# Kernel optimization log

Measured on AMD Instinct MI355X. Metric: run time of the kernel, lower is better.

The kernel has to match this reference:

```python
import jax, jax.numpy as jnp
import numpy as np

B, H, S, D = 2, 16, 2048, 64  # batch, heads, seq (n_qry == n_tok), head_dim


def setup_inputs() -> dict:
    key = jax.random.key(0)
    kq, kk, kv = jax.random.split(key, 3)
    Q = jax.random.normal(kq, (B, H, S, D), dtype=jnp.float32)
    K_cache = jax.random.normal(kk, (B, H, S, D), dtype=jnp.float32)
    V_cache = jax.random.normal(kv, (B, H, S, D), dtype=jnp.float32)
    return {"Q": Q, "K_cache": K_cache, "V_cache": V_cache}


def reference(Q, K_cache, V_cache):
    n_qry = Q.shape[-2]
    n_tok = K_cache.shape[-2]
    scale = 1.0 / jnp.sqrt(jnp.asarray(Q.shape[-1], Q.dtype))
    # [B, H, n_qry, n_tok] scores
    A = jnp.einsum('bhqd,bhkd->bhqk', Q, K_cache) * scale
    # causal mask: query q may attend key k iff k <= q + (n_tok - n_qry)
    q_idx = jnp.arange(n_qry)[:, None]
    k_idx = jnp.arange(n_tok)[None, :]
    mask = k_idx <= q_idx + (n_tok - n_qry)
    A = jnp.where(mask, A, -jnp.inf)
    P = jax.nn.softmax(A, axis=-1)
    return jnp.einsum('bhqk,bhkd->bhqd', P, V_cache)
```

## Files before the change

kernel.cpp:

```cpp
#include <hip/hip_runtime.h>

typedef __attribute__((ext_vector_type(8))) short bf16x8;
typedef __attribute__((ext_vector_type(4))) short bf16x4;
typedef __attribute__((ext_vector_type(4))) float f32x4;

#define NB 2
#define NH 16
#define NS 2048
#define ND 64
#define NBH (NB * NH)
#define QSCALE (0.125f * 1.44269504088896f)
#define CMAX 12.0f

static __device__ __forceinline__ unsigned pack2(float lo, float hi) {
  return __builtin_amdgcn_perm(__builtin_bit_cast(unsigned, hi),
                               __builtin_bit_cast(unsigned, lo), 0x07060302u);
}

__global__ __launch_bounds__(256) void prep_kernel(const float* __restrict__ K,
                                                   const float* __restrict__ V,
                                                   short* __restrict__ W) {
  const int bh = blockIdx.x >> 5, kb = blockIdx.x & 31;
  const float* Kp = K + (size_t)bh * NS * ND + (size_t)kb * 64 * ND;
  const float* Vp = V + (size_t)bh * NS * ND + (size_t)kb * 64 * ND;
  short* Wp = W + ((size_t)bh * 32 + kb) * 8192;

#pragma unroll
  for (int e0 = 0; e0 < 512; e0 += 256) {
    int e = e0 + threadIdx.x;
    int c = e >> 6, lane = e & 63;
    int st = c >> 1, cc = c & 1, quad = lane >> 4, col = lane & 15;
    const float* kr = Kp + (st * 16 + col) * ND + cc * 32 + quad * 8;
    float4 a = *(const float4*)kr;
    float4 b = *(const float4*)(kr + 4);
    uint4 u = {pack2(a.x, a.y), pack2(a.z, a.w), pack2(b.x, b.y), pack2(b.z, b.w)};
    *(uint4*)(Wp + (size_t)e * 8) = u;
  }
#pragma unroll
  for (int e0 = 0; e0 < 512; e0 += 256) {
    int e = e0 + threadIdx.x;
    int c = e >> 6, lane = e & 63;
    int st = c >> 1, th = c & 1, quad = lane >> 4, col = lane & 15;
    float f[8];
#pragma unroll
    for (int r = 0; r < 8; ++r) {
      int j = r & 3, t = th * 2 + (r >> 2);
      f[r] = Vp[(st * 16 + quad * 4 + j) * ND + t * 16 + col];
    }
    uint4 u = {pack2(f[0], f[1]), pack2(f[2], f[3]),
               pack2(f[4], f[5]), pack2(f[6], f[7])};
    *(uint4*)(Wp + 4096 + (size_t)e * 8) = u;
  }
}

__global__ __launch_bounds__(256) void fa_kernel(
    const float* __restrict__ Q, const short* __restrict__ W,
    float* __restrict__ O) {
  const int lane = threadIdx.x & 63;
  const int wave = threadIdx.x >> 6;
  const int col  = lane & 15;
  const int quad = lane >> 4;
  const int xcd  = blockIdx.x & 7;
  const int slot = blockIdx.x >> 3;
  const int bh   = xcd * 4 + (slot >> 4);
  const int pr   = slot & 15;
  const int stepsA = pr + 1;
  const int tileB  = 31 - pr;
  const int TOT = 33;

  __shared__ short Kbuf[2][4096];
  __shared__ short Vbuf[2][4096];

  const float* Qp = Q + (size_t)bh * NS * ND;
  const short* Wb = W + (size_t)bh * 32 * 8192;
  float*       Op = O + (size_t)bh * NS * ND;

  bf16x8 qf[2];
  f32x4 o4[4];
  float lsum;

  auto loadQ = [&](int qtile) {
    const float* qrow = Qp + (size_t)(qtile * 64 + wave * 16 + col) * ND + quad * 8;
#pragma unroll
    for (int c = 0; c < 2; ++c) {
      float4 a = *(const float4*)(qrow + c * 32);
      float4 b = *(const float4*)(qrow + c * 32 + 4);
      union { bf16x8 v; unsigned u[4]; } t;
      t.u[0] = pack2(a.x * QSCALE, a.y * QSCALE);
      t.u[1] = pack2(a.z * QSCALE, a.w * QSCALE);
      t.u[2] = pack2(b.x * QSCALE, b.y * QSCALE);
      t.u[3] = pack2(b.z * QSCALE, b.w * QSCALE);
      qf[c] = t.v;
    }
#pragma unroll
    for (int t = 0; t < 4; ++t) o4[t] = (f32x4){0.f, 0.f, 0.f, 0.f};
    lsum = 0.f;
  };

  auto stage = [&](int s, int b) {
    int kt = (s < stepsA) ? s : s - stepsA;
    const short* base = Wb + (size_t)kt * 8192;
#pragma unroll
    for (int i = 0; i < 4; ++i) {
      int id = wave * 4 + i;
      const short* g = base + id * 512 + lane * 8;
      __attribute__((address_space(3))) void* dst =
          (id < 8)
              ? (__attribute__((address_space(3))) void*)&Kbuf[b][id * 512]
              : (__attribute__((address_space(3))) void*)&Vbuf[b][(id - 8) * 512];
      __builtin_amdgcn_global_load_lds(
          (const __attribute__((address_space(1))) void*)g, dst, 16, 0, 0);
    }
  };

  auto epilogue = [&](int qtile) {
    float lt = lsum;
    lt += __shfl_xor(lt, 16, 64);
    lt += __shfl_xor(lt, 32, 64);
#pragma unroll
    for (int r = 0; r < 4; ++r) {
      float lr = __shfl(lt, quad * 4 + r, 64);
      float inv = 1.0f / lr;
      float* orow = Op + (size_t)(qtile * 64 + wave * 16 + quad * 4 + r) * ND + col;
#pragma unroll
      for (int t = 0; t < 4; ++t) orow[t * 16] = o4[t][r] * inv;
    }
  };

  loadQ(pr);
  stage(0, 0);
  __syncthreads();

  int qtile = pr;
  bool inB = false;
  for (int s = 0; s < TOT; ++s) {
    if (s + 1 < TOT) stage(s + 1, (s + 1) & 1);
    const int b = s & 1;
    const int local = inB ? (s - stepsA) : s;
    const int steps = inB ? (32 - pr) : stepsA;
    const bool last = (local == steps - 1);

    float sc[4][4];
#pragma unroll
    for (int st = 0; st < 4; ++st) {
      bf16x8 k0 = *(const bf16x8*)&Kbuf[b][(st * 2 + 0) * 512 + lane * 8];
      bf16x8 k1 = *(const bf16x8*)&Kbuf[b][(st * 2 + 1) * 512 + lane * 8];
      f32x4 acc = (f32x4){-CMAX, -CMAX, -CMAX, -CMAX};
      acc = __builtin_amdgcn_mfma_f32_16x16x32_bf16(k0, qf[0], acc, 0, 0, 0);
      acc = __builtin_amdgcn_mfma_f32_16x16x32_bf16(k1, qf[1], acc, 0, 0, 0);
#pragma unroll
      for (int r = 0; r < 4; ++r) sc[st][r] = acc[r];
    }
    if (last) {
      int qo = wave * 16 + col;
#pragma unroll
      for (int st = 0; st < 4; ++st)
#pragma unroll
        for (int r = 0; r < 4; ++r)
          if (st * 16 + quad * 4 + r > qo) sc[st][r] = -INFINITY;
    }

    bf16x4 pf[4];
#pragma unroll
    for (int st = 0; st < 4; ++st) {
      float p0 = __builtin_amdgcn_exp2f(sc[st][0]);
      float p1 = __builtin_amdgcn_exp2f(sc[st][1]);
      float p2 = __builtin_amdgcn_exp2f(sc[st][2]);
      float p3 = __builtin_amdgcn_exp2f(sc[st][3]);
      lsum += (p0 + p1) + (p2 + p3);
      union { bf16x4 v; unsigned u[2]; } tp;
      tp.u[0] = pack2(p0, p1);
      tp.u[1] = pack2(p2, p3);
      pf[st] = tp.v;
    }

#pragma unroll
    for (int st = 0; st < 4; ++st)
#pragma unroll
      for (int th = 0; th < 2; ++th) {
        bf16x8 vv = *(const bf16x8*)&Vbuf[b][(st * 2 + th) * 512 + lane * 8];
        bf16x4 vlo = __builtin_shufflevector(vv, vv, 0, 1, 2, 3);
        bf16x4 vhi = __builtin_shufflevector(vv, vv, 4, 5, 6, 7);
        o4[th * 2 + 0] =
            __builtin_amdgcn_mfma_f32_16x16x16bf16_1k(pf[st], vlo, o4[th * 2 + 0], 0, 0, 0);
        o4[th * 2 + 1] =
            __builtin_amdgcn_mfma_f32_16x16x16bf16_1k(pf[st], vhi, o4[th * 2 + 1], 0, 0, 0);
      }

    if (last) {
      epilogue(qtile);
      if (!inB) { inB = true; qtile = tileB; loadQ(tileB); }
    }
    __syncthreads();
  }
}

extern "C" void kernel_launch(void* const* d_in, const int* in_sizes, int n_in,
                              void* d_out, int out_size, void* d_ws, size_t ws_size,
                              hipStream_t stream) {
  const float* Q = (const float*)d_in[0];
  const float* K = (const float*)d_in[1];
  const float* V = (const float*)d_in[2];
  short* W = (short*)d_ws;
  hipLaunchKernelGGL(prep_kernel, dim3(NBH * 32), dim3(256), 0, stream, K, V, W);
  hipLaunchKernelGGL(fa_kernel, dim3(512), dim3(256), 0, stream, Q, W,
                     (float*)d_out);
}
```

Measured before the change: 123.6 us.

## Process paired query tiles concurrently per block with 16x16x32 PV MFMAs

Each block now runs its two causal query tiles concurrently: waves 0-1 handle the short tile and waves 2-3 the long tile. Each wave covers 32 query rows, so every K/V LDS fragment is reused across two MFMAs. The K and V workspace layout is permuted so the PV product can use 16x16x32 bf16 MFMAs instead of 16x16x16. V is transposed through padded shared memory in the prep kernel, and the grid is reordered into two phases with launch_bounds(256,2). The waves on the short tile sit idle after finishing, which trades load balance within a block for fewer loop steps and fewer LDS reads per FLOP.

```diff
diff --git a/kernel.cpp b/kernel.cpp
--- a/kernel.cpp
+++ b/kernel.cpp
@@ -1,14 +1,13 @@
 #include <hip/hip_runtime.h>
 
 typedef __attribute__((ext_vector_type(8))) short bf16x8;
-typedef __attribute__((ext_vector_type(4))) short bf16x4;
 typedef __attribute__((ext_vector_type(4))) float f32x4;
 
 #define NB 2
 #define NH 16
 #define NS 2048
 #define ND 64
-#define NBH (NB * NH)
+#define NBH 32
 #define QSCALE (0.125f * 1.44269504088896f)
 #define CMAX 12.0f
 
@@ -16,6 +15,7 @@
   return __builtin_amdgcn_perm(__builtin_bit_cast(unsigned, hi),
                                __builtin_bit_cast(unsigned, lo), 0x07060302u);
 }
+
 
 __global__ __launch_bounds__(256) void prep_kernel(const float* __restrict__ K,
                                                    const float* __restrict__ V,
@@ -25,48 +25,70 @@
   const float* Vp = V + (size_t)bh * NS * ND + (size_t)kb * 64 * ND;
   short* Wp = W + ((size_t)bh * 32 + kb) * 8192;
 
+  __shared__ float vt[64 * 65];
+
+  {
+    int vrow = threadIdx.x >> 2, seg = threadIdx.x & 3;
+    const float* src = Vp + vrow * ND + seg * 16;
+    float* dst = vt + vrow * 65 + seg * 16;
+#pragma unroll
+    for (int i = 0; i < 4; ++i) {
+      float4 v = *(const float4*)(src + i * 4);
+      dst[i * 4 + 0] = v.x; dst[i * 4 + 1] = v.y;
+      dst[i * 4 + 2] = v.z; dst[i * 4 + 3] = v.w;
+    }
+  }
+
 #pragma unroll
   for (int e0 = 0; e0 < 512; e0 += 256) {
     int e = e0 + threadIdx.x;
     int c = e >> 6, lane = e & 63;
     int st = c >> 1, cc = c & 1, quad = lane >> 4, col = lane & 15;
-    const float* kr = Kp + (st * 16 + col) * ND + cc * 32 + quad * 8;
+    int prow = 32 * (st >> 1) + 8 * (col >> 2) + 4 * (st & 1) + (col & 3);
+    const float* kr = Kp + prow * ND + cc * 32 + quad * 8;
     float4 a = *(const float4*)kr;
     float4 b = *(const float4*)(kr + 4);
     uint4 u = {pack2(a.x, a.y), pack2(a.z, a.w), pack2(b.x, b.y), pack2(b.z, b.w)};
     *(uint4*)(Wp + (size_t)e * 8) = u;
   }
+  __syncthreads();
+
 #pragma unroll
   for (int e0 = 0; e0 < 512; e0 += 256) {
     int e = e0 + threadIdx.x;
     int c = e >> 6, lane = e & 63;
-    int st = c >> 1, th = c & 1, quad = lane >> 4, col = lane & 15;
+    int g = c >> 2, t = c & 3, quad = lane >> 4, col = lane & 15;
+    const float* base = vt + (32 * g + 8 * quad) * 65 + t * 16 + col;
     float f[8];
 #pragma unroll
-    for (int r = 0; r < 8; ++r) {
-      int j = r & 3, t = th * 2 + (r >> 2);
-      f[r] = Vp[(st * 16 + quad * 4 + j) * ND + t * 16 + col];
-    }
+    for (int j = 0; j < 8; ++j) f[j] = base[j * 65];
     uint4 u = {pack2(f[0], f[1]), pack2(f[2], f[3]),
                pack2(f[4], f[5]), pack2(f[6], f[7])};
     *(uint4*)(Wp + 4096 + (size_t)e * 8) = u;
   }
 }
 
-__global__ __launch_bounds__(256) void fa_kernel(
+__global__ __launch_bounds__(256, 2) void fa_kernel(
     const float* __restrict__ Q, const short* __restrict__ W,
     float* __restrict__ O) {
   const int lane = threadIdx.x & 63;
   const int wave = threadIdx.x >> 6;
   const int col  = lane & 15;
   const int quad = lane >> 4;
-  const int xcd  = blockIdx.x & 7;
-  const int slot = blockIdx.x >> 3;
-  const int bh   = xcd * 4 + (slot >> 4);
-  const int pr   = slot & 15;
+
+  const int i = blockIdx.x;
+  const int phase = i >> 8;
+  const int rr_ = i & 255;
+  const int xcd = rr_ & 7;
+  const int s5 = rr_ >> 3;
+  const int bh = xcd * 4 + (s5 & 3);
+  const int pp = s5 >> 2;
+  const int pr = phase ? (15 - pp) : pp;
   const int stepsA = pr + 1;
-  const int tileB  = 31 - pr;
-  const int TOT = 33;
+  const int TOT = 32 - pr;
+  const int myTile  = (wave < 2) ? pr : (31 - pr);
+  const int mySteps = (wave < 2) ? stepsA : TOT;
+  const int qhalf = wave & 1;
 
   __shared__ short Kbuf[2][4096];
   __shared__ short Vbuf[2][4096];
@@ -75,12 +97,11 @@
   const short* Wb = W + (size_t)bh * 32 * 8192;
   float*       Op = O + (size_t)bh * NS * ND;
 
-  bf16x8 qf[2];
-  f32x4 o4[4];
-  float lsum;
-
-  auto loadQ = [&](int qtile) {
-    const float* qrow = Qp + (size_t)(qtile * 64 + wave * 16 + col) * ND + quad * 8;
+  bf16x8 qf[2][2];
+#pragma unroll
+  for (int f = 0; f < 2; ++f) {
+    const float* qrow =
+        Qp + (size_t)(myTile * 64 + qhalf * 32 + f * 16 + col) * ND + quad * 8;
 #pragma unroll
     for (int c = 0; c < 2; ++c) {
       float4 a = *(const float4*)(qrow + c * 32);
@@ -90,19 +111,22 @@
       t.u[1] = pack2(a.z * QSCALE, a.w * QSCALE);
       t.u[2] = pack2(b.x * QSCALE, b.y * QSCALE);
       t.u[3] = pack2(b.z * QSCALE, b.w * QSCALE);
-      qf[c] = t.v;
-    }
-#pragma unroll
-    for (int t = 0; t < 4; ++t) o4[t] = (f32x4){0.f, 0.f, 0.f, 0.f};
-    lsum = 0.f;
-  };
+      qf[f][c] = t.v;
+    }
+  }
+
+  f32x4 o4[2][4];
+#pragma unroll
+  for (int f = 0; f < 2; ++f)
+#pragma unroll
+    for (int t = 0; t < 4; ++t) o4[f][t] = (f32x4){0.f, 0.f, 0.f, 0.f};
+  float lsum[2] = {0.f, 0.f};
 
   auto stage = [&](int s, int b) {
-    int kt = (s < stepsA) ? s : s - stepsA;
-    const short* base = Wb + (size_t)kt * 8192;
-#pragma unroll
-    for (int i = 0; i < 4; ++i) {
-      int id = wave * 4 + i;
+    const short* base = Wb + (size_t)s * 8192;
+#pragma unroll
+    for (int ii = 0; ii < 4; ++ii) {
+      int id = wave * 4 + ii;
       const short* g = base + id * 512 + lane * 8;
       __attribute__((address_space(3))) void* dst =
           (id < 8)
@@ -113,83 +137,95 @@
     }
   };
 
-  auto epilogue = [&](int qtile) {
-    float lt = lsum;
-    lt += __shfl_xor(lt, 16, 64);
-    lt += __shfl_xor(lt, 32, 64);
-#pragma unroll
-    for (int r = 0; r < 4; ++r) {
-      float lr = __shfl(lt, quad * 4 + r, 64);
-      float inv = 1.0f / lr;
-      float* orow = Op + (size_t)(qtile * 64 + wave * 16 + quad * 4 + r) * ND + col;
-#pragma unroll
-      for (int t = 0; t < 4; ++t) orow[t * 16] = o4[t][r] * inv;
-    }
-  };
-
-  loadQ(pr);
   stage(0, 0);
   __syncthreads();
 
-  int qtile = pr;
-  bool inB = false;
   for (int s = 0; s < TOT; ++s) {
     if (s + 1 < TOT) stage(s + 1, (s + 1) & 1);
     const int b = s & 1;
-    const int local = inB ? (s - stepsA) : s;
-    const int steps = inB ? (32 - pr) : stepsA;
-    const bool last = (local == steps - 1);
-
-    float sc[4][4];
-#pragma unroll
-    for (int st = 0; st < 4; ++st) {
-      bf16x8 k0 = *(const bf16x8*)&Kbuf[b][(st * 2 + 0) * 512 + lane * 8];
-      bf16x8 k1 = *(const bf16x8*)&Kbuf[b][(st * 2 + 1) * 512 + lane * 8];
-      f32x4 acc = (f32x4){-CMAX, -CMAX, -CMAX, -CMAX};
-      acc = __builtin_amdgcn_mfma_f32_16x16x32_bf16(k0, qf[0], acc, 0, 0, 0);
-      acc = __builtin_amdgcn_mfma_f32_16x16x32_bf16(k1, qf[1], acc, 0, 0, 0);
-#pragma unroll
-      for (int r = 0; r < 4; ++r) sc[st][r] = acc[r];
-    }
-    if (last) {
-      int qo = wave * 16 + col;
-#pragma unroll
-      for (int st = 0; st < 4; ++st)
-#pragma unroll
-        for (int r = 0; r < 4; ++r)
-          if (st * 16 + quad * 4 + r > qo) sc[st][r] = -INFINITY;
-    }
-
-    bf16x4 pf[4];
-#pragma unroll
-    for (int st = 0; st < 4; ++st) {
-      float p0 = __builtin_amdgcn_exp2f(sc[st][0]);
-      float p1 = __builtin_amdgcn_exp2f(sc[st][1]);
-      float p2 = __builtin_amdgcn_exp2f(sc[st][2]);
-      float p3 = __builtin_amdgcn_exp2f(sc[st][3]);
-      lsum += (p0 + p1) + (p2 + p3);
-      union { bf16x4 v; unsigned u[2]; } tp;
-      tp.u[0] = pack2(p0, p1);
-      tp.u[1] = pack2(p2, p3);
-      pf[st] = tp.v;
-    }
-
-#pragma unroll
-    for (int st = 0; st < 4; ++st)
-#pragma unroll
-      for (int th = 0; th < 2; ++th) {
-        bf16x8 vv = *(const bf16x8*)&Vbuf[b][(st * 2 + th) * 512 + lane * 8];
-        bf16x4 vlo = __builtin_shufflevector(vv, vv, 0, 1, 2, 3);
-        bf16x4 vhi = __builtin_shufflevector(vv, vv, 4, 5, 6, 7);
-        o4[th * 2 + 0] =
-            __builtin_amdgcn_mfma_f32_16x16x16bf16_1k(pf[st], vlo, o4[th * 2 + 0], 0, 0, 0);
-        o4[th * 2 + 1] =
-            __builtin_amdgcn_mfma_f32_16x16x16bf16_1k(pf[st], vhi, o4[th * 2 + 1], 0, 0, 0);
+
+    if (s < mySteps) {
+      const bool last = (s == mySteps - 1);
+
+      float sc[2][4][4];
+#pragma unroll
+      for (int st = 0; st < 4; ++st) {
+        bf16x8 k0 = *(const bf16x8*)&Kbuf[b][(st * 2 + 0) * 512 + lane * 8];
+        bf16x8 k1 = *(const bf16x8*)&Kbuf[b][(st * 2 + 1) * 512 + lane * 8];
+#pragma unroll
+        for (int f = 0; f < 2; ++f) {
+          f32x4 acc = (f32x4){-CMAX, -CMAX, -CMAX, -CMAX};
+          acc = __builtin_amdgcn_mfma_f32_16x16x32_bf16(k0, qf[f][0], acc, 0, 0, 0);
+          acc = __builtin_amdgcn_mfma_f32_16x16x32_bf16(k1, qf[f][1], acc, 0, 0, 0);
+#pragma unroll
+          for (int r = 0; r < 4; ++r) sc[f][st][r] = acc[r];
+        }
       }
 
-    if (last) {
-      epilogue(qtile);
-      if (!inB) { inB = true; qtile = tileB; loadQ(tileB); }
+      if (last) {
+#pragma unroll
+        for (int f = 0; f < 2; ++f) {
+          int qin = qhalf * 32 + f * 16 + col;
+#pragma unroll
+          for (int st = 0; st < 4; ++st)
+#pragma unroll
+            for (int r = 0; r < 4; ++r) {
+              int phys = 32 * (st >> 1) + 8 * quad + 4 * (st & 1) + r;
+              if (phys > qin) sc[f][st][r] = -INFINITY;
+            }
+        }
+      }
+
+      bf16x8 pf[2][2];
+#pragma unroll
+      for (int f = 0; f < 2; ++f)
+#pragma unroll
+        for (int g = 0; g < 2; ++g) {
+          float p0 = __builtin_amdgcn_exp2f(sc[f][2 * g + 0][0]);
+          float p1 = __builtin_amdgcn_exp2f(sc[f][2 * g + 0][1]);
+          float p2 = __builtin_amdgcn_exp2f(sc[f][2 * g + 0][2]);
+          float p3 = __builtin_amdgcn_exp2f(sc[f][2 * g + 0][3]);
+          float p4 = __builtin_amdgcn_exp2f(sc[f][2 * g + 1][0]);
+          float p5 = __builtin_amdgcn_exp2f(sc[f][2 * g + 1][1]);
+          float p6 = __builtin_amdgcn_exp2f(sc[f][2 * g + 1][2]);
+          float p7 = __builtin_amdgcn_exp2f(sc[f][2 * g + 1][3]);
+          lsum[f] += ((p0 + p1) + (p2 + p3)) + ((p4 + p5) + (p6 + p7));
+          union { bf16x8 v; unsigned u[4]; } t;
+          t.u[0] = pack2(p0, p1);
+          t.u[1] = pack2(p2, p3);
+          t.u[2] = pack2(p4, p5);
+          t.u[3] = pack2(p6, p7);
+          pf[f][g] = t.v;
+        }
+
+#pragma unroll
+      for (int g = 0; g < 2; ++g)
+#pragma unroll
+        for (int t = 0; t < 4; ++t) {
+          bf16x8 vf = *(const bf16x8*)&Vbuf[b][(g * 4 + t) * 512 + lane * 8];
+#pragma unroll
+          for (int f = 0; f < 2; ++f)
+            o4[f][t] = __builtin_amdgcn_mfma_f32_16x16x32_bf16(pf[f][g], vf,
+                                                               o4[f][t], 0, 0, 0);
+        }
+
+      if (last) {
+#pragma unroll
+        for (int f = 0; f < 2; ++f) {
+          float lt = lsum[f];
+          lt += __shfl_xor(lt, 16, 64);
+          lt += __shfl_xor(lt, 32, 64);
+#pragma unroll
+          for (int r = 0; r < 4; ++r) {
+            float lr = __shfl(lt, quad * 4 + r, 64);
+            float inv = 1.0f / lr;
+            float* orow = Op + (size_t)(myTile * 64 + qhalf * 32 + f * 16 +
+                                        quad * 4 + r) * ND + col;
+#pragma unroll
+            for (int t = 0; t < 4; ++t) orow[t * 16] = o4[f][t][r] * inv;
+          }
+        }
+      }
     }
     __syncthreads();
   }
```

Measured after the change: 125.4 us. About the same (+1.4%).
